# Optimization experiments

Measured on AMD Instinct MI355X. Metric: run time of the kernel, lower is better.

The kernel has to match this reference:

```python
import jax, jax.numpy as jnp
import numpy as np

STRIDE = 4
NUM_HEADS = 8


def _make_window(x, stride, nh):
    # (B,C,H,W) -> (B, nh, S, S, (H/S)*(W/S), C/nh)
    b, c, h, w = x.shape
    x = x.reshape(b, nh, c // nh, h // stride, stride, w // stride, stride)
    x = x.transpose(0, 1, 4, 6, 3, 5, 2)
    return x.reshape(b, nh, stride, stride, (h // stride) * (w // stride), c // nh)


def _demake_window(x, h, w):
    # (B, nh, S, S, L, dh) -> (B, nh*dh, H, W)
    b, nh, s, _, L, dh = x.shape
    x = x.reshape(b, nh, s, s, h // s, w // s, dh)
    x = x.transpose(0, 1, 6, 4, 2, 5, 3)
    return x.reshape(b, nh * dh, h, w)


def _proj(x, W, bias):
    # 1x1 conv == per-pixel GEMM: (B,C,H,W),(O,C) -> (B,O,H,W)
    return jnp.einsum('bchw,oc->bohw', x, W) + bias[None, :, None, None]


def setup_inputs() -> dict:
    key = jax.random.key(0)
    ks = jax.random.split(key, 12)
    B, C, H, W = 4, 256, 64, 64
    P, V, O = 256, 256, 256  # proj/value/out channels
    inp = {
        'fea_q': jax.random.normal(ks[0], (B, C, H, W), jnp.float32),
        'fea_k': jax.random.normal(ks[1], (B, C, H, W), jnp.float32),
        'fea_v': jax.random.normal(ks[2], (B, V, H, W), jnp.float32),
        'mask_q': (jax.random.uniform(ks[3], (B, 1, H, W)) > 0.5).astype(jnp.float32),
        'mask_k': (jax.random.uniform(ks[4], (B, 1, H, W)) > 0.5).astype(jnp.float32),
        'q_w': jax.random.normal(ks[5], (P, C), jnp.float32) * 0.02,
        'q_b': jnp.zeros((P,), jnp.float32),
        'k_w': jax.random.normal(ks[6], (P, C), jnp.float32) * 0.02,
        'k_b': jnp.zeros((P,), jnp.float32),
        'v_w': jax.random.normal(ks[7], (O, V), jnp.float32) * 0.02,
        'v_b': jnp.zeros((O,), jnp.float32),
    }
    return inp


def reference(fea_q, fea_k, fea_v, mask_q, mask_k, q_w, q_b, k_w, k_b, v_w, v_b):
    B, _, H, W = fea_q.shape
    head_dim = q_w.shape[0] // NUM_HEADS
    scaling = head_dim ** (-0.5)

    query = _make_window(_proj(fea_q, q_w, q_b), STRIDE, NUM_HEADS)
    key = _make_window(_proj(fea_k, k_w, k_b), STRIDE, NUM_HEADS)
    value = _make_window(_proj(fea_v, v_w, v_b), STRIDE, NUM_HEADS)

    # (B, nh, S, S, L, L)
    weights = jnp.matmul(query, jnp.swapaxes(key, -1, -2)) * scaling

    # mask attention (no-grad in original)
    mq = _make_window(jax.lax.stop_gradient(mask_q), STRIDE, 1)
    mk = _make_window(jax.lax.stop_gradient(mask_k), STRIDE, 1)
    mask_attn = jnp.matmul(mq, jnp.swapaxes(mk, -1, -2))  # (B,1,S,S,L,L)
    mask_sum = jnp.sum(mask_attn, axis=-1, keepdims=True)
    mask_attn = mask_attn + (mask_sum == 0).astype(jnp.float32)
    mask_attn = jnp.where(mask_attn == 0, -jnp.inf,
                          jnp.where(mask_attn == 1, 0.0, mask_attn))
    weights = weights + mask_attn

    weights = jax.nn.softmax(weights, axis=-1)  # dropout p=0 -> identity
    weights = weights * (1.0 - (mask_sum == 0).astype(jnp.float32))

    out = jnp.matmul(weights, value)  # (B, nh, S, S, L, dh)
    return _demake_window(out, H, W)
```

## Files before the change

### kernel.cpp

```cpp
#include <hip/hip_runtime.h>

#define NH 8
#define DH 32
#define LW 256
#define HW 4096
#define CIN 256

typedef float f32x4 __attribute__((ext_vector_type(4)));
typedef short s16x8 __attribute__((ext_vector_type(8)));
typedef short s16x4 __attribute__((ext_vector_type(4)));

#define AS1 __attribute__((address_space(1)))
#define AS3 __attribute__((address_space(3)))

__device__ __forceinline__ short f2bf(float f) {
  unsigned u; __builtin_memcpy(&u, &f, 4);
  u = (u + 0x7FFFu + ((u >> 16) & 1u)) >> 16;
  return (short)u;
}

__device__ __forceinline__ void gload_lds16(const void* g, void* l) {
  __builtin_amdgcn_global_load_lds((const AS1 void*)g, (AS3 void*)l, 16, 0, 0);
}

#define KOFF 4194304
#define VOFF 8388608

__global__ void __launch_bounds__(256, 3)
proj_kernel(const float* __restrict__ fq, const float* __restrict__ fk,
            const float* __restrict__ fv,
            const float* __restrict__ qw, const float* __restrict__ qb,
            const float* __restrict__ kw, const float* __restrict__ kb_,
            const float* __restrict__ vw, const float* __restrict__ vb,
            short* __restrict__ ws) {
  __shared__ s16x8 SMEM[2048];
  s16x8* AsV = SMEM;
  s16x8* BsV = SMEM + 1024;

  int bid = blockIdx.x;
  int orig = (bid & 7) * 96 + (bid >> 3);
  int t = orig >> 8;
  int r0 = orig & 255;
  int b = r0 >> 6;
  int pblk = (r0 >> 1) & 31;
  int oblk = r0 & 1;

  const float* fea = (t == 0) ? fq : ((t == 1) ? fk : fv);
  const float* Wm  = (t == 0) ? qw : ((t == 1) ? kw : vw);
  const float* Bv  = (t == 0) ? qb : ((t == 1) ? kb_ : vb);

  int p0 = pblk * 128, o0 = oblk * 128;
  int tid = threadIdx.x;
  int lane = tid & 63, wv = tid >> 6;
  int g = lane >> 4, li = lane & 15;

  const f32x4 fzero = {0.f, 0.f, 0.f, 0.f};
  f32x4 acc[2][8];
#pragma unroll
  for (int m = 0; m < 2; ++m)
#pragma unroll
    for (int n = 0; n < 8; ++n) acc[m][n] = fzero;

  const float* feab = fea + b * (CIN * HW);
  int coct = tid >> 5;
  int pq = (tid & 31) * 4;

  f32x4 ldA[8];
  f32x4 ldB[8];

#define LOAD_A(cs_) do { int c0_ = (cs_) * 64; _Pragma("unroll") \
  for (int i_ = 0; i_ < 4; ++i_) { int ch_ = i_ * 256 + tid; int o_ = ch_ >> 3, kb2_ = ch_ & 7; \
    const float* s_ = Wm + (o0 + o_) * CIN + c0_ + kb2_ * 8; \
    ldA[2 * i_] = *(const f32x4*)s_; ldA[2 * i_ + 1] = *(const f32x4*)(s_ + 4); } } while (0)

#define LOAD_B(cs_) do { int c0_ = (cs_) * 64; _Pragma("unroll") \
  for (int j_ = 0; j_ < 8; ++j_) \
    ldB[j_] = *(const f32x4*)(feab + (c0_ + coct * 8 + j_) * HW + p0 + pq); } while (0)

  LOAD_A(0);
  LOAD_B(0);

  for (int cs = 0; cs < 4; ++cs) {
    __syncthreads();
#pragma unroll
    for (int i = 0; i < 4; ++i) {
      int ch = i * 256 + tid;
      int o = ch >> 3, kb2 = ch & 7;
      s16x8 v;
#pragma unroll
      for (int j = 0; j < 4; ++j) { v[j] = f2bf(ldA[2 * i][j]); v[4 + j] = f2bf(ldA[2 * i + 1][j]); }
      AsV[o * 8 + (kb2 ^ (o & 7))] = v;
    }
#pragma unroll
    for (int pp = 0; pp < 4; ++pp) {
      s16x8 v;
#pragma unroll
      for (int j = 0; j < 8; ++j) v[j] = f2bf(ldB[j][pp]);
      int p = pq + pp;
      int pidx = p ^ ((p >> 3) & 7);
      BsV[coct * 128 + pidx] = v;
    }
    __syncthreads();
    if (cs < 3) { LOAD_A(cs + 1); LOAD_B(cs + 1); }
#pragma unroll
    for (int kk = 0; kk < 2; ++kk) {
      int or0 = wv * 32 + li;
      int or1 = or0 + 16;
      s16x8 a0 = AsV[or0 * 8 + ((kk * 4 + g) ^ (or0 & 7))];
      s16x8 a1 = AsV[or1 * 8 + ((kk * 4 + g) ^ (or1 & 7))];
#pragma unroll
      for (int n = 0; n < 8; ++n) {
        int p = n * 16 + li;
        int pidx = p ^ ((p >> 3) & 7);
        s16x8 bb = BsV[(kk * 4 + g) * 128 + pidx];
        acc[0][n] = __builtin_amdgcn_mfma_f32_16x16x32_bf16(a0, bb, acc[0][n], 0, 0, 0);
        acc[1][n] = __builtin_amdgcn_mfma_f32_16x16x32_bf16(a1, bb, acc[1][n], 0, 0, 0);
      }
    }
  }
#undef LOAD_A
#undef LOAD_B

  float bias_r[2][4];
#pragma unroll
  for (int m = 0; m < 2; ++m)
#pragma unroll
    for (int rr = 0; rr < 4; ++rr)
      bias_r[m][rr] = Bv[o0 + wv * 32 + m * 16 + g * 4 + rr];

  if (t != 2) {
    int nh = oblk * 4 + wv;
#pragma unroll
    for (int m = 0; m < 2; ++m) {
      int kb = m * 2 + (g >> 1);
      int dlo = (g & 1) * 4;
#pragma unroll
      for (int n = 0; n < 8; ++n) {
        int p = p0 + n * 16 + li;
        int h = p >> 6, w = p & 63;
        int s1 = h & 3, h0 = h >> 2, s2 = w & 3, w0 = w >> 2;
        int wwin = s1 * 4 + s2, l = h0 * 16 + w0;
        int winbase = (b * NH + nh) * 16 + wwin;
        s16x4 v;
#pragma unroll
        for (int rr = 0; rr < 4; ++rr) v[rr] = f2bf(acc[m][n][rr] + bias_r[m][rr]);
        short* dst = ws + (t == 0 ? 0 : KOFF);
        *(s16x4*)(dst + winbase * 8192 + (kb * 256 + l) * 8 + dlo) = v;
      }
    }
  } else {
    __syncthreads();
    short* Tr = (short*)SMEM;
#pragma unroll
    for (int m = 0; m < 2; ++m) {
      int ob = wv * 32 + m * 16 + g * 4;
#pragma unroll
      for (int n = 0; n < 8; ++n) {
        int p = n * 16 + li;
        s16x4 v;
#pragma unroll
        for (int rr = 0; rr < 4; ++rr) v[rr] = f2bf(acc[m][n][rr] + bias_r[m][rr]);
        *(s16x4*)(Tr + p * 128 + (ob ^ ((p & 15) << 2))) = v;
      }
    }
    __syncthreads();
    int d128 = tid >> 1;
    int h_idx = tid & 1;
    int nh2 = (o0 + d128) >> 5, d = (o0 + d128) & 31;
    int hh = (p0 >> 6) + h_idx;
    int s1e = hh & 3, h0e = hh >> 2;
#pragma unroll
    for (int j = 0; j < 8; ++j) {
      int s2e = j & 3, woct = j >> 2;
      s16x8 v;
#pragma unroll
      for (int k = 0; k < 8; ++k) {
        int pl = h_idx * 64 + s2e + 32 * woct + 4 * k;
        v[k] = Tr[pl * 128 + (d128 ^ ((pl & 15) << 2))];
      }
      int wwin = s1e * 4 + s2e;
      int l_oct = h0e * 2 + woct;
      int winbase = (b * NH + nh2) * 16 + wwin;
      *(s16x8*)(ws + VOFF + winbase * 8192 + d * 256 + l_oct * 8) = v;
    }
  }
}

__global__ void __launch_bounds__(256, 4)
attn_kernel(const short* __restrict__ ws, const float* __restrict__ mq,
            const float* __restrict__ mk, float* __restrict__ out) {
  __shared__ s16x8 KsV[1024];
  __shared__ s16x8 PsV[512];
  __shared__ float amaskS[256];
  __shared__ float mqS[128];
  __shared__ float facS[128];
  __shared__ int anyS[4];

  int bid = blockIdx.x;
  int orig = (bid & 7) * 128 + (bid >> 3);
  int qh = orig & 1;
  int s2 = (orig >> 1) & 3, s1 = (orig >> 3) & 3, nh = (orig >> 5) & 7, b = orig >> 8;
  int wwin = s1 * 4 + s2;
  int tid = threadIdx.x;
  int lane = tid & 63, wv = tid >> 6, g = lane >> 4, li = lane & 15;

  int winbase = (b * NH + nh) * 16 + wwin;
  const short* qt = ws + winbase * 8192;
  const short* kt = ws + KOFF + winbase * 8192;
  const short* vt = ws + VOFF + winbase * 8192;

#pragma unroll
  for (int i = 0; i < 4; ++i) {
    int seg = i * 4 + wv;
    gload_lds16(kt + (seg * 64 + lane) * 8, &KsV[seg * 64]);
  }

  {
    int l = tid;
    int h = (l >> 4) * 4 + s1, w = (l & 15) * 4 + s2;
    float mkv = mk[b * HW + h * 64 + w];
    amaskS[l] = (mkv > 0.5f) ? 0.0f : -1e30f;
    unsigned long long bal = __ballot(mkv > 0.5f);
    if (lane == 0) anyS[wv] = (bal != 0ULL) ? 1 : 0;
  }
  if (tid < 128) {
    int l = qh * 128 + tid;
    int h = (l >> 4) * 4 + s1, w = (l & 15) * 4 + s2;
    mqS[tid] = mq[b * HW + h * 64 + w];
  }

  int lq0 = wv * 32;
  s16x8 qa[2];
#pragma unroll
  for (int m = 0; m < 2; ++m)
    qa[m] = *(const s16x8*)(qt + (g * 256 + qh * 128 + lq0 + m * 16 + li) * 8);

  __syncthreads();
  int anyk = anyS[0] | anyS[1] | anyS[2] | anyS[3];

  const f32x4 fzero = {0.f, 0.f, 0.f, 0.f};
  f32x4 of[2][2];
#pragma unroll
  for (int m = 0; m < 2; ++m) { of[m][0] = fzero; of[m][1] = fzero; }
  float rs[8];
#pragma unroll
  for (int i = 0; i < 8; ++i) rs[i] = 0.0f;

  const float scaling = 0.17677669529663689f;

#pragma unroll
  for (int lkb = 0; lkb < 4; ++lkb) {
    f32x4 sa[2][4];
#pragma unroll
    for (int n = 0; n < 4; ++n) {
      s16x8 kf = KsV[g * 256 + lkb * 64 + n * 16 + li];
#pragma unroll
      for (int m = 0; m < 2; ++m)
        sa[m][n] = __builtin_amdgcn_mfma_f32_16x16x32_bf16(qa[m], kf, fzero, 0, 0, 0);
    }
#pragma unroll
    for (int ks = 0; ks < 2; ++ks) {
#pragma unroll
      for (int n2 = 0; n2 < 2; ++n2) {
        int n = ks * 2 + n2;
        float am = amaskS[lkb * 64 + n * 16 + li];
#pragma unroll
        for (int m = 0; m < 2; ++m) {
#pragma unroll
          for (int rr = 0; rr < 4; ++rr) {
            float pval = __expf(sa[m][n][rr] * scaling + am);
            rs[m * 4 + rr] += pval;
            int row = m * 16 + g * 4 + rr;
            int cl = n * 16 + li;
            int kbh = (cl >> 3) & 3;
            short* ps = (short*)&PsV[wv * 128 + kbh * 32 + row];
            ps[cl & 7] = f2bf(pval);
          }
        }
      }
      int kg = lkb * 2 + ks;
      s16x8 pb[2];
#pragma unroll
      for (int n = 0; n < 2; ++n) pb[n] = PsV[wv * 128 + g * 32 + n * 16 + li];
#pragma unroll
      for (int m2 = 0; m2 < 2; ++m2) {
        s16x8 va = *(const s16x8*)(vt + (m2 * 16 + li) * 256 + (kg * 4 + g) * 8);
#pragma unroll
        for (int n = 0; n < 2; ++n)
          of[m2][n] = __builtin_amdgcn_mfma_f32_16x16x32_bf16(va, pb[n], of[m2][n], 0, 0, 0);
      }
    }
  }

#pragma unroll
  for (int i = 0; i < 8; ++i) {
    float v = rs[i];
    v += __shfl_xor(v, 1);
    v += __shfl_xor(v, 2);
    v += __shfl_xor(v, 4);
    v += __shfl_xor(v, 8);
    rs[i] = v;
  }
  if (li == 0) {
#pragma unroll
    for (int m = 0; m < 2; ++m)
#pragma unroll
      for (int rr = 0; rr < 4; ++rr) {
        int row = m * 16 + g * 4 + rr;
        float sum = rs[m * 4 + rr];
        facS[wv * 32 + row] = (anyk && mqS[wv * 32 + row] > 0.5f) ? (1.0f / sum) : 0.0f;
      }
  }

#pragma unroll
  for (int m2 = 0; m2 < 2; ++m2) {
#pragma unroll
    for (int n = 0; n < 2; ++n) {
      int lloc = wv * 32 + n * 16;
      float fac = facS[lloc + li];
      int l = qh * 128 + lloc;
      int h = (l >> 4) * 4 + s1;
      int w = li * 4 + s2;
#pragma unroll
      for (int rr = 0; rr < 4; ++rr) {
        int o = nh * 32 + m2 * 16 + g * 4 + rr;
        out[((b * 256 + o) * 64 + h) * 64 + w] = of[m2][n][rr] * fac;
      }
    }
  }
}

extern "C" void kernel_launch(void* const* d_in, const int* in_sizes, int n_in,
                              void* d_out, int out_size, void* d_ws, size_t ws_size,
                              hipStream_t stream) {
  const float* fq = (const float*)d_in[0];
  const float* fk = (const float*)d_in[1];
  const float* fv = (const float*)d_in[2];
  const float* mq = (const float*)d_in[3];
  const float* mk = (const float*)d_in[4];
  const float* qw = (const float*)d_in[5];
  const float* qb = (const float*)d_in[6];
  const float* kw = (const float*)d_in[7];
  const float* kb = (const float*)d_in[8];
  const float* vw = (const float*)d_in[9];
  const float* vb = (const float*)d_in[10];
  short* ws = (short*)d_ws;

  proj_kernel<<<768, 256, 0, stream>>>(fq, fk, fv, qw, qb, kw, kb, vw, vb, ws);
  attn_kernel<<<1024, 256, 0, stream>>>(ws, mq, mk, (float*)d_out);
}
```

Before: 47.94 us.

## Pre-convert projection weights to bf16 and double-buffer feature tiles in LDS

Adds a small kernel that converts the Q/K/V weight matrices to bf16 once per call, in an MFMA-friendly blocked layout. The projection GEMM then reads A fragments straight from global memory instead of converting and staging them in LDS in every block. The feature tile is double-buffered in LDS, which cuts the loop to one barrier per step. The softmax exponent now uses exp2f with log2(e) folded into the scale, and f2bf uses the HIP bf16 intrinsic. The cost is an extra kernel launch, plus uncached-in-LDS global reads of the weights on the MFMA critical path.

```diff
diff --git a/kernel.cpp b/kernel.cpp
--- a/kernel.cpp
+++ b/kernel.cpp
@@ -1,4 +1,5 @@
 #include <hip/hip_runtime.h>
+#include <hip/hip_bf16.h>
 
 #define NH 8
 #define DH 32
@@ -14,9 +15,8 @@
 #define AS3 __attribute__((address_space(3)))
 
 __device__ __forceinline__ short f2bf(float f) {
-  unsigned u; __builtin_memcpy(&u, &f, 4);
-  u = (u + 0x7FFFu + ((u >> 16) & 1u)) >> 16;
-  return (short)u;
+  __hip_bfloat16 h = __float2bfloat16(f);
+  short s; __builtin_memcpy(&s, &h, 2); return s;
 }
 
 __device__ __forceinline__ void gload_lds16(const void* g, void* l) {
@@ -25,17 +25,29 @@
 
 #define KOFF 4194304
 #define VOFF 8388608
+#define WTOFF 12582912
+
+__global__ void wconv_kernel(const float* __restrict__ qw, const float* __restrict__ kw,
+                             const float* __restrict__ vw, short* __restrict__ ws) {
+  int blk = blockIdx.x;
+  int t = blk >> 5, kb = blk & 31;
+  const float* W = (t == 0) ? qw : ((t == 1) ? kw : vw);
+  int o = threadIdx.x;
+  f32x4 w0 = *(const f32x4*)(W + o * CIN + kb * 8);
+  f32x4 w1 = *(const f32x4*)(W + o * CIN + kb * 8 + 4);
+  s16x8 v;
+#pragma unroll
+  for (int j = 0; j < 4; ++j) { v[j] = f2bf(w0[j]); v[4 + j] = f2bf(w1[j]); }
+  *(s16x8*)(ws + WTOFF + (blk * 256 + o) * 8) = v;
+}
 
 __global__ void __launch_bounds__(256, 3)
 proj_kernel(const float* __restrict__ fq, const float* __restrict__ fk,
             const float* __restrict__ fv,
-            const float* __restrict__ qw, const float* __restrict__ qb,
-            const float* __restrict__ kw, const float* __restrict__ kb_,
-            const float* __restrict__ vw, const float* __restrict__ vb,
+            const float* __restrict__ qb, const float* __restrict__ kb_,
+            const float* __restrict__ vb,
             short* __restrict__ ws) {
   __shared__ s16x8 SMEM[2048];
-  s16x8* AsV = SMEM;
-  s16x8* BsV = SMEM + 1024;
 
   int bid = blockIdx.x;
   int orig = (bid & 7) * 96 + (bid >> 3);
@@ -46,8 +58,8 @@
   int oblk = r0 & 1;
 
   const float* fea = (t == 0) ? fq : ((t == 1) ? fk : fv);
-  const float* Wm  = (t == 0) ? qw : ((t == 1) ? kw : vw);
   const float* Bv  = (t == 0) ? qb : ((t == 1) ? kb_ : vb);
+  const short* Wt  = ws + WTOFF + t * 65536;
 
   int p0 = pblk * 128, o0 = oblk * 128;
   int tid = threadIdx.x;
@@ -65,61 +77,46 @@
   int coct = tid >> 5;
   int pq = (tid & 31) * 4;
 
-  f32x4 ldA[8];
   f32x4 ldB[8];
-
-#define LOAD_A(cs_) do { int c0_ = (cs_) * 64; _Pragma("unroll") \
-  for (int i_ = 0; i_ < 4; ++i_) { int ch_ = i_ * 256 + tid; int o_ = ch_ >> 3, kb2_ = ch_ & 7; \
-    const float* s_ = Wm + (o0 + o_) * CIN + c0_ + kb2_ * 8; \
-    ldA[2 * i_] = *(const f32x4*)s_; ldA[2 * i_ + 1] = *(const f32x4*)(s_ + 4); } } while (0)
 
 #define LOAD_B(cs_) do { int c0_ = (cs_) * 64; _Pragma("unroll") \
   for (int j_ = 0; j_ < 8; ++j_) \
     ldB[j_] = *(const f32x4*)(feab + (c0_ + coct * 8 + j_) * HW + p0 + pq); } while (0)
 
-  LOAD_A(0);
+#define WRITE_B(buf_) do { _Pragma("unroll") \
+  for (int pp_ = 0; pp_ < 4; ++pp_) { s16x8 v_; _Pragma("unroll") \
+    for (int j_ = 0; j_ < 8; ++j_) v_[j_] = f2bf(ldB[j_][pp_]); \
+    int p_ = pq + pp_; int pidx_ = p_ ^ ((p_ >> 3) & 7); \
+    SMEM[(buf_) * 1024 + coct * 128 + pidx_] = v_; } } while (0)
+
   LOAD_B(0);
+  WRITE_B(0);
+  __syncthreads();
 
   for (int cs = 0; cs < 4; ++cs) {
-    __syncthreads();
-#pragma unroll
-    for (int i = 0; i < 4; ++i) {
-      int ch = i * 256 + tid;
-      int o = ch >> 3, kb2 = ch & 7;
-      s16x8 v;
-#pragma unroll
-      for (int j = 0; j < 4; ++j) { v[j] = f2bf(ldA[2 * i][j]); v[4 + j] = f2bf(ldA[2 * i + 1][j]); }
-      AsV[o * 8 + (kb2 ^ (o & 7))] = v;
-    }
-#pragma unroll
-    for (int pp = 0; pp < 4; ++pp) {
-      s16x8 v;
-#pragma unroll
-      for (int j = 0; j < 8; ++j) v[j] = f2bf(ldB[j][pp]);
-      int p = pq + pp;
-      int pidx = p ^ ((p >> 3) & 7);
-      BsV[coct * 128 + pidx] = v;
-    }
-    __syncthreads();
-    if (cs < 3) { LOAD_A(cs + 1); LOAD_B(cs + 1); }
+    if (cs < 3) LOAD_B(cs + 1);
 #pragma unroll
     for (int kk = 0; kk < 2; ++kk) {
-      int or0 = wv * 32 + li;
-      int or1 = or0 + 16;
-      s16x8 a0 = AsV[or0 * 8 + ((kk * 4 + g) ^ (or0 & 7))];
-      s16x8 a1 = AsV[or1 * 8 + ((kk * 4 + g) ^ (or1 & 7))];
+      int kbg = cs * 8 + kk * 4 + g;
+      const short* abase = Wt + (kbg * 256 + o0 + wv * 32 + li) * 8;
+      s16x8 a0 = *(const s16x8*)(abase);
+      s16x8 a1 = *(const s16x8*)(abase + 128);
 #pragma unroll
       for (int n = 0; n < 8; ++n) {
         int p = n * 16 + li;
         int pidx = p ^ ((p >> 3) & 7);
-        s16x8 bb = BsV[(kk * 4 + g) * 128 + pidx];
+        s16x8 bb = SMEM[(cs & 1) * 1024 + (kk * 4 + g) * 128 + pidx];
         acc[0][n] = __builtin_amdgcn_mfma_f32_16x16x32_bf16(a0, bb, acc[0][n], 0, 0, 0);
         acc[1][n] = __builtin_amdgcn_mfma_f32_16x16x32_bf16(a1, bb, acc[1][n], 0, 0, 0);
       }
     }
-  }
-#undef LOAD_A
+    if (cs < 3) {
+      WRITE_B((cs + 1) & 1);
+      __syncthreads();
+    }
+  }
 #undef LOAD_B
+#undef WRITE_B
 
   float bias_r[2][4];
 #pragma unroll
@@ -246,7 +243,7 @@
 #pragma unroll
   for (int i = 0; i < 8; ++i) rs[i] = 0.0f;
 
-  const float scaling = 0.17677669529663689f;
+  const float C = 0.17677669529663689f * 1.4426950408889634f;
 
 #pragma unroll
   for (int lkb = 0; lkb < 4; ++lkb) {
@@ -268,7 +265,7 @@
         for (int m = 0; m < 2; ++m) {
 #pragma unroll
           for (int rr = 0; rr < 4; ++rr) {
-            float pval = __expf(sa[m][n][rr] * scaling + am);
+            float pval = exp2f(sa[m][n][rr] * C + am);
             rs[m * 4 + rr] += pval;
             int row = m * 16 + g * 4 + rr;
             int cl = n * 16 + li;
@@ -346,6 +343,7 @@
   const float* vb = (const float*)d_in[10];
   short* ws = (short*)d_ws;
 
-  proj_kernel<<<768, 256, 0, stream>>>(fq, fk, fv, qw, qb, kw, kb, vw, vb, ws);
+  wconv_kernel<<<96, 256, 0, stream>>>(qw, kw, vw, ws);
+  proj_kernel<<<768, 256, 0, stream>>>(fq, fk, fv, qb, kb, vb, ws);
   attn_kernel<<<1024, 256, 0, stream>>>(ws, mq, mk, (float*)d_out);
 }
```

After: 51.92 us. 8.3% more time.

## Halve projection output tile to double grid and occupancy; use exp2 softmax

Applied to the files above, without the earlier changes.

The projection GEMM now gives each block a 64-output-channel by 128-pixel tile instead of 128 by 128. This doubles the grid to 1536 blocks, cuts the LDS footprint and accumulators, and raises the launch-bounds occupancy target from 3 to 4. The V-transpose epilogue is reworked to match the smaller tile. In exchange, each input feature tile is now loaded by four blocks instead of two, which adds global/L2 read traffic. Separately, the attention softmax folds log2(e) into the scale and uses exp2f, and bf16 conversion now uses the HIP intrinsic.

```diff
diff --git a/kernel.cpp b/kernel.cpp
--- a/kernel.cpp
+++ b/kernel.cpp
@@ -1,4 +1,5 @@
 #include <hip/hip_runtime.h>
+#include <hip/hip_bf16.h>
 
 #define NH 8
 #define DH 32
@@ -14,9 +15,8 @@
 #define AS3 __attribute__((address_space(3)))
 
 __device__ __forceinline__ short f2bf(float f) {
-  unsigned u; __builtin_memcpy(&u, &f, 4);
-  u = (u + 0x7FFFu + ((u >> 16) & 1u)) >> 16;
-  return (short)u;
+  __hip_bfloat16 h = __float2bfloat16(f);
+  short s; __builtin_memcpy(&s, &h, 2); return s;
 }
 
 __device__ __forceinline__ void gload_lds16(const void* g, void* l) {
@@ -26,50 +26,48 @@
 #define KOFF 4194304
 #define VOFF 8388608
 
-__global__ void __launch_bounds__(256, 3)
+__global__ void __launch_bounds__(256, 4)
 proj_kernel(const float* __restrict__ fq, const float* __restrict__ fk,
             const float* __restrict__ fv,
             const float* __restrict__ qw, const float* __restrict__ qb,
             const float* __restrict__ kw, const float* __restrict__ kb_,
             const float* __restrict__ vw, const float* __restrict__ vb,
             short* __restrict__ ws) {
-  __shared__ s16x8 SMEM[2048];
+  __shared__ s16x8 SMEM[1536];
   s16x8* AsV = SMEM;
-  s16x8* BsV = SMEM + 1024;
+  s16x8* BsV = SMEM + 512;
 
   int bid = blockIdx.x;
-  int orig = (bid & 7) * 96 + (bid >> 3);
-  int t = orig >> 8;
-  int r0 = orig & 255;
-  int b = r0 >> 6;
-  int pblk = (r0 >> 1) & 31;
-  int oblk = r0 & 1;
+  int orig = (bid & 7) * 192 + (bid >> 3);
+  int t = orig >> 9;
+  int r0 = orig & 511;
+  int b = r0 >> 7;
+  int pblk = (r0 >> 2) & 31;
+  int oblk = r0 & 3;
 
   const float* fea = (t == 0) ? fq : ((t == 1) ? fk : fv);
   const float* Wm  = (t == 0) ? qw : ((t == 1) ? kw : vw);
   const float* Bv  = (t == 0) ? qb : ((t == 1) ? kb_ : vb);
 
-  int p0 = pblk * 128, o0 = oblk * 128;
+  int p0 = pblk * 128, o0 = oblk * 64;
   int tid = threadIdx.x;
   int lane = tid & 63, wv = tid >> 6;
   int g = lane >> 4, li = lane & 15;
 
   const f32x4 fzero = {0.f, 0.f, 0.f, 0.f};
-  f32x4 acc[2][8];
-#pragma unroll
-  for (int m = 0; m < 2; ++m)
-#pragma unroll
-    for (int n = 0; n < 8; ++n) acc[m][n] = fzero;
+  f32x4 acc[8];
+#pragma unroll
+  for (int n = 0; n < 8; ++n) acc[n] = fzero;
 
   const float* feab = fea + b * (CIN * HW);
   int coct = tid >> 5;
   int pq = (tid & 31) * 4;
 
-  f32x4 ldA[8];
+  f32x4 ldA[4];
   f32x4 ldB[8];
 
 #define LOAD_A(cs_) do { int c0_ = (cs_) * 64; _Pragma("unroll") \
-  for (int i_ = 0; i_ < 4; ++i_) { int ch_ = i_ * 256 + tid; int o_ = ch_ >> 3, kb2_ = ch_ & 7; \
+  for (int i_ = 0; i_ < 2; ++i_) { int ch_ = i_ * 256 + tid; int o_ = ch_ >> 3, kb2_ = ch_ & 7; \
     const float* s_ = Wm + (o0 + o_) * CIN + c0_ + kb2_ * 8; \
     ldA[2 * i_] = *(const f32x4*)s_; ldA[2 * i_ + 1] = *(const f32x4*)(s_ + 4); } } while (0)
 
@@ -77,106 +75,92 @@
   for (int j_ = 0; j_ < 8; ++j_) \
     ldB[j_] = *(const f32x4*)(feab + (c0_ + coct * 8 + j_) * HW + p0 + pq); } while (0)
 
+#define WRITE_AB() do { _Pragma("unroll") \
+  for (int i_ = 0; i_ < 2; ++i_) { int ch_ = i_ * 256 + tid; int o_ = ch_ >> 3, kb2_ = ch_ & 7; \
+    s16x8 v_; _Pragma("unroll") \
+    for (int j_ = 0; j_ < 4; ++j_) { v_[j_] = f2bf(ldA[2 * i_][j_]); v_[4 + j_] = f2bf(ldA[2 * i_ + 1][j_]); } \
+    AsV[o_ * 8 + (kb2_ ^ (o_ & 7))] = v_; } \
+  _Pragma("unroll") \
+  for (int pp_ = 0; pp_ < 4; ++pp_) { s16x8 v_; _Pragma("unroll") \
+    for (int j_ = 0; j_ < 8; ++j_) v_[j_] = f2bf(ldB[j_][pp_]); \
+    int p_ = pq + pp_; int pidx_ = p_ ^ ((p_ >> 3) & 7); \
+    BsV[coct * 128 + pidx_] = v_; } } while (0)
+
   LOAD_A(0);
   LOAD_B(0);
 
   for (int cs = 0; cs < 4; ++cs) {
     __syncthreads();
-#pragma unroll
-    for (int i = 0; i < 4; ++i) {
-      int ch = i * 256 + tid;
-      int o = ch >> 3, kb2 = ch & 7;
-      s16x8 v;
-#pragma unroll
-      for (int j = 0; j < 4; ++j) { v[j] = f2bf(ldA[2 * i][j]); v[4 + j] = f2bf(ldA[2 * i + 1][j]); }
-      AsV[o * 8 + (kb2 ^ (o & 7))] = v;
-    }
-#pragma unroll
-    for (int pp = 0; pp < 4; ++pp) {
-      s16x8 v;
-#pragma unroll
-      for (int j = 0; j < 8; ++j) v[j] = f2bf(ldB[j][pp]);
-      int p = pq + pp;
-      int pidx = p ^ ((p >> 3) & 7);
-      BsV[coct * 128 + pidx] = v;
-    }
+    WRITE_AB();
     __syncthreads();
     if (cs < 3) { LOAD_A(cs + 1); LOAD_B(cs + 1); }
 #pragma unroll
     for (int kk = 0; kk < 2; ++kk) {
-      int or0 = wv * 32 + li;
-      int or1 = or0 + 16;
+      int or0 = wv * 16 + li;
       s16x8 a0 = AsV[or0 * 8 + ((kk * 4 + g) ^ (or0 & 7))];
-      s16x8 a1 = AsV[or1 * 8 + ((kk * 4 + g) ^ (or1 & 7))];
 #pragma unroll
       for (int n = 0; n < 8; ++n) {
         int p = n * 16 + li;
         int pidx = p ^ ((p >> 3) & 7);
         s16x8 bb = BsV[(kk * 4 + g) * 128 + pidx];
-        acc[0][n] = __builtin_amdgcn_mfma_f32_16x16x32_bf16(a0, bb, acc[0][n], 0, 0, 0);
-        acc[1][n] = __builtin_amdgcn_mfma_f32_16x16x32_bf16(a1, bb, acc[1][n], 0, 0, 0);
+        acc[n] = __builtin_amdgcn_mfma_f32_16x16x32_bf16(a0, bb, acc[n], 0, 0, 0);
       }
     }
   }
 #undef LOAD_A
 #undef LOAD_B
-
-  float bias_r[2][4];
-#pragma unroll
-  for (int m = 0; m < 2; ++m)
-#pragma unroll
-    for (int rr = 0; rr < 4; ++rr)
-      bias_r[m][rr] = Bv[o0 + wv * 32 + m * 16 + g * 4 + rr];
+#undef WRITE_AB
+
+  int od = o0 + wv * 16 + g * 4;
+  float bias_r[4];
+#pragma unroll
+  for (int rr = 0; rr < 4; ++rr) bias_r[rr] = Bv[od + rr];
 
   if (t != 2) {
-    int nh = oblk * 4 + wv;
-#pragma unroll
-    for (int m = 0; m < 2; ++m) {
-      int kb = m * 2 + (g >> 1);
-      int dlo = (g & 1) * 4;
-#pragma unroll
-      for (int n = 0; n < 8; ++n) {
-        int p = p0 + n * 16 + li;
-        int h = p >> 6, w = p & 63;
-        int s1 = h & 3, h0 = h >> 2, s2 = w & 3, w0 = w >> 2;
-        int wwin = s1 * 4 + s2, l = h0 * 16 + w0;
-        int winbase = (b * NH + nh) * 16 + wwin;
-        s16x4 v;
-#pragma unroll
-        for (int rr = 0; rr < 4; ++rr) v[rr] = f2bf(acc[m][n][rr] + bias_r[m][rr]);
-        short* dst = ws + (t == 0 ? 0 : KOFF);
-        *(s16x4*)(dst + winbase * 8192 + (kb * 256 + l) * 8 + dlo) = v;
-      }
+    int nh = od >> 5;
+    int kb = (od & 31) >> 3;
+    int dlo = od & 7;
+#pragma unroll
+    for (int n = 0; n < 8; ++n) {
+      int p = p0 + n * 16 + li;
+      int h = p >> 6, w = p & 63;
+      int s1 = h & 3, h0 = h >> 2, s2 = w & 3, w0 = w >> 2;
+      int wwin = s1 * 4 + s2, l = h0 * 16 + w0;
+      int winbase = (b * NH + nh) * 16 + wwin;
+      s16x4 v;
+#pragma unroll
+      for (int rr = 0; rr < 4; ++rr) v[rr] = f2bf(acc[n][rr] + bias_r[rr]);
+      short* dst = ws + (t == 0 ? 0 : KOFF);
+      *(s16x4*)(dst + winbase * 8192 + (kb * 256 + l) * 8 + dlo) = v;
     }
   } else {
     __syncthreads();
     short* Tr = (short*)SMEM;
-#pragma unroll
-    for (int m = 0; m < 2; ++m) {
-      int ob = wv * 32 + m * 16 + g * 4;
-#pragma unroll
-      for (int n = 0; n < 8; ++n) {
-        int p = n * 16 + li;
-        s16x4 v;
-#pragma unroll
-        for (int rr = 0; rr < 4; ++rr) v[rr] = f2bf(acc[m][n][rr] + bias_r[m][rr]);
-        *(s16x4*)(Tr + p * 128 + (ob ^ ((p & 15) << 2))) = v;
-      }
+    int ob = wv * 16 + g * 4;
+#pragma unroll
+    for (int n = 0; n < 8; ++n) {
+      int p = n * 16 + li;
+      s16x4 v;
+#pragma unroll
+      for (int rr = 0; rr < 4; ++rr) v[rr] = f2bf(acc[n][rr] + bias_r[rr]);
+      *(s16x4*)(Tr + p * 64 + (ob ^ ((p & 15) << 2))) = v;
     }
     __syncthreads();
-    int d128 = tid >> 1;
-    int h_idx = tid & 1;
-    int nh2 = (o0 + d128) >> 5, d = (o0 + d128) & 31;
+    int o_local = tid >> 2;
+    int sub = tid & 3;
+    int h_idx = sub >> 1;
+    int woct = sub & 1;
+    int o = o0 + o_local;
+    int nh2 = o >> 5, d = o & 31;
     int hh = (p0 >> 6) + h_idx;
     int s1e = hh & 3, h0e = hh >> 2;
 #pragma unroll
-    for (int j = 0; j < 8; ++j) {
-      int s2e = j & 3, woct = j >> 2;
+    for (int s2e = 0; s2e < 4; ++s2e) {
       s16x8 v;
 #pragma unroll
       for (int k = 0; k < 8; ++k) {
         int pl = h_idx * 64 + s2e + 32 * woct + 4 * k;
-        v[k] = Tr[pl * 128 + (d128 ^ ((pl & 15) << 2))];
+        v[k] = Tr[pl * 64 + (o_local ^ ((pl & 15) << 2))];
       }
       int wwin = s1e * 4 + s2e;
       int l_oct = h0e * 2 + woct;
@@ -246,7 +230,7 @@
 #pragma unroll
   for (int i = 0; i < 8; ++i) rs[i] = 0.0f;
 
-  const float scaling = 0.17677669529663689f;
+  const float C = 0.17677669529663689f * 1.4426950408889634f;
 
 #pragma unroll
   for (int lkb = 0; lkb < 4; ++lkb) {
@@ -268,7 +252,7 @@
         for (int m = 0; m < 2; ++m) {
 #pragma unroll
           for (int rr = 0; rr < 4; ++rr) {
-            float pval = __expf(sa[m][n][rr] * scaling + am);
+            float pval = exp2f(sa[m][n][rr] * C + am);
             rs[m * 4 + rr] += pval;
             int row = m * 16 + g * 4 + rr;
             int cl = n * 16 + li;
@@ -346,6 +330,6 @@
   const float* vb = (const float*)d_in[10];
   short* ws = (short*)d_ws;
 
-  proj_kernel<<<768, 256, 0, stream>>>(fq, fk, fv, qw, qb, kw, kb, vw, vb, ws);
+  proj_kernel<<<1536, 256, 0, stream>>>(fq, fk, fv, qw, qb, kw, kb, vw, vb, ws);
   attn_kernel<<<1024, 256, 0, stream>>>(ws, mq, mk, (float*)d_out);
 }
```

Measured after the change: 48.70 us. About the same (+1.6%).
